# Performance work log

Measured on AMD Instinct MI355X. Metric: run time of the kernel, lower is better.

Reference implementation:

```python
import jax, jax.numpy as jnp
import numpy as np

N, F_IN, H, P, R = 50000, 384, 128, 128, 16
E = 500000


def _lin_params(key, fan_in, fan_out):
    k1, k2 = jax.random.split(key)
    s = 1.0 / np.sqrt(fan_in)
    W = jax.random.uniform(k1, (fan_in, fan_out), jnp.float32, -s, s)
    b = jax.random.uniform(k2, (fan_out,), jnp.float32, -s, s)
    return W, b


def setup_inputs() -> dict:
    key = jax.random.key(0)
    ks = jax.random.split(key, 16)
    x = jax.random.normal(ks[0], (N, F_IN), jnp.float32)
    edge_index = jax.random.randint(ks[1], (2, E), 0, N, jnp.int64)
    W_gcn1, b_gcn1 = _lin_params(ks[2], F_IN, H)
    W_ti, b_ti = _lin_params(ks[3], F_IN, F_IN)      # CrossFusion.text_info (384 -> dim=384)
    W_gi, b_gi = _lin_params(ks[4], H, F_IN)          # CrossFusion.graph_info (128 -> 384)
    W_v, b_v = _lin_params(ks[5], F_IN, F_IN)         # CrossFusion.value
    Wl1, bl1 = _lin_params(ks[6], F_IN, F_IN // 2)    # left_generator hidden
    Wl2, bl2 = _lin_params(ks[7], F_IN // 2, P * R)
    Wr1, br1 = _lin_params(ks[8], F_IN, F_IN // 2)    # right_generator hidden
    Wr2, br2 = _lin_params(ks[9], F_IN // 2, R * F_IN)
    W_gcn2, b_gcn2 = _lin_params(ks[10], P, H)        # fusion_gcn (128 -> 128)
    W_gp, b_gp = _lin_params(ks[11], P, P)            # graph_proj
    return dict(x=x, edge_index=edge_index, W_gcn1=W_gcn1, b_gcn1=b_gcn1,
                W_ti=W_ti, b_ti=b_ti, W_gi=W_gi, b_gi=b_gi, W_v=W_v, b_v=b_v,
                Wl1=Wl1, bl1=bl1, Wl2=Wl2, bl2=bl2, Wr1=Wr1, br1=br1, Wr2=Wr2, br2=br2,
                W_gcn2=W_gcn2, b_gcn2=b_gcn2, W_gp=W_gp, b_gp=b_gp)


def _gcn(x, W, b, src, dst, n):
    # PyG GCNConv: self-loops + symmetric degree normalization, aggregate at dst.
    xw = x @ W
    loop = jnp.arange(n, dtype=src.dtype)
    s = jnp.concatenate([src, loop])
    d = jnp.concatenate([dst, loop])
    deg = jax.ops.segment_sum(jnp.ones_like(d, dtype=xw.dtype), d, num_segments=n)
    dinv = jnp.where(deg > 0, jax.lax.rsqrt(deg), 0.0)
    norm = dinv[s] * dinv[d]                           # [E+N]
    out = jax.ops.segment_sum(norm[:, None] * xw[s], d, num_segments=n)
    return out + b


def _cross_fusion(text_feat, graph_feat, row, col, W_ti, b_ti, W_gi, b_gi, W_v, b_v):
    n, dim = text_feat.shape[0], W_ti.shape[1]
    t_info = text_feat @ W_ti + b_ti                   # [N, dim]
    g_info = graph_feat @ W_gi + b_gi                  # [N, dim]
    v = text_feat @ W_v + b_v                          # [N, dim]
    scores = jnp.sum(t_info[row] * g_info[col], axis=-1) / np.sqrt(dim)   # [E]
    m = jax.ops.segment_max(scores, row, num_segments=n)                  # scatter_softmax
    e = jnp.exp(scores - m[row])
    denom = jax.ops.segment_sum(e, row, num_segments=n)
    attn = e / denom[row]
    out = jax.ops.segment_sum(attn[:, None] * v[col], row, num_segments=n)
    return out + text_feat


def _forward(x, edge_index, W_gcn1, b_gcn1, W_ti, b_ti, W_gi, b_gi, W_v, b_v,
             Wl1, bl1, Wl2, bl2, Wr1, br1, Wr2, br2, W_gcn2, b_gcn2, W_gp, b_gp):
    src, dst = edge_index[0], edge_index[1]
    n = x.shape[0]
    g_emb = _gcn(x, W_gcn1, b_gcn1, src, dst, n)
    x_fused = _cross_fusion(x, g_emb, src, dst, W_ti, b_ti, W_gi, b_gi, W_v, b_v)
    # N > 40000 -> low-rank chunked projection (chunking is pure batching; vectorize)
    left = (jax.nn.relu(x_fused @ Wl1 + bl1) @ Wl2 + bl2).reshape(n, P, R)
    right = (jax.nn.relu(x_fused @ Wr1 + br1) @ Wr2 + br2).reshape(n, R, F_IN)
    temp = jnp.einsum('nrf,nf->nr', right, x)
    p_t = jnp.einsum('npr,nr->np', left, temp)         # [N, P]
    g2 = _gcn(p_t, W_gcn2, b_gcn2, src, dst, n)        # dropout is identity in eval
    p_g = g2 @ W_gp + b_gp
    p_t = p_t / jnp.maximum(jnp.linalg.norm(p_t, axis=-1, keepdims=True), 1e-12)
    p_g = p_g / jnp.maximum(jnp.linalg.norm(p_g, axis=-1, keepdims=True), 1e-12)
    alignment = jnp.sum(p_t * p_g, axis=1)
    return alignment, p_t, p_g, g2


def reference(x, edge_index, W_gcn1, b_gcn1, W_ti, b_ti, W_gi, b_gi, W_v, b_v,
              Wl1, bl1, Wl2, bl2, Wr1, br1, Wr2, br2, W_gcn2, b_gcn2, W_gp, b_gp):
    return _forward(x, edge_index, W_gcn1, b_gcn1, W_ti, b_ti, W_gi, b_gi, W_v, b_v,
                    Wl1, bl1, Wl2, bl2, Wr1, br1, Wr2, br2, W_gcn2, b_gcn2, W_gp, b_gp)
```

## Files before the change

kernel.cpp:

```cpp
#include <hip/hip_runtime.h>

typedef unsigned int u32;
typedef unsigned short u16;
typedef short s16x8 __attribute__((ext_vector_type(8)));
typedef u16 u16x8 __attribute__((ext_vector_type(8)));
typedef float f32x4 __attribute__((ext_vector_type(4)));

#define FIN 384
#define HD  128
#define PD  128
#define RD  16

#define GLOAD16(g, l)                                                          \
  __builtin_amdgcn_global_load_lds(                                            \
      (const __attribute__((address_space(1))) void*)(g),                      \
      (__attribute__((address_space(3))) void*)(l), 16, 0, 0)

__device__ __forceinline__ u16 f2bf(float f) {
  u32 u = __float_as_uint(f);
  u32 r = (u + 0x7fffu + ((u >> 16) & 1u)) >> 16;
  return (u16)r;
}
__device__ __forceinline__ float bf2f(u16 h) {
  return __uint_as_float(((u32)h) << 16);
}

struct CvtEnt { const float* s; u16* d; int K, N, mode, blk0; };
struct CvtDesc { CvtEnt e[12]; int n; };

__global__ void cvt_all_k(CvtDesc dsc) {
  int b = blockIdx.x;
  int ei = 0;
  while (ei + 1 < dsc.n && dsc.e[ei + 1].blk0 <= b) ++ei;
  CvtEnt E = dsc.e[ei];
  int i = (b - E.blk0) * 256 + (int)threadIdx.x;
  int tot = E.K * E.N;
  if (i >= tot) return;
  float v;
  if (E.mode == 0) {
    int c = i / E.K, k = i - c * E.K;
    v = E.s[(size_t)k * E.N + c];
  } else if (E.mode == 1) {
    v = E.s[i];
  } else {
    int q = i / 384, f = i - q * 384;
    v = E.s[(size_t)(q >> 4) * 6144 + (q & 15) * 384 + f];
  }
  E.d[i] = f2bf(v);
}

__global__ void hist_k(const int* __restrict__ src, const int* __restrict__ dst,
                       u32* __restrict__ cnt, int n, int E) {
  int i = blockIdx.x * 256 + threadIdx.x;
  if (i < E) {
    atomicAdd(&cnt[src[i]], 1u);
    atomicAdd(&cnt[n + dst[i]], 1u);
  }
}

__global__ __launch_bounds__(1024)
void scanA_k(const u32* __restrict__ cnt, u32* __restrict__ off,
             u32* __restrict__ bsum, int n2) {
  __shared__ u32 sh[1024];
  int i = blockIdx.x * 1024 + (int)threadIdx.x;
  u32 v = (i < n2) ? cnt[i] : 0u;
  sh[threadIdx.x] = v;
  __syncthreads();
  for (int s = 1; s < 1024; s <<= 1) {
    u32 t = (threadIdx.x >= (u32)s) ? sh[threadIdx.x - s] : 0u;
    __syncthreads();
    sh[threadIdx.x] += t;
    __syncthreads();
  }
  if (i < n2) off[i] = sh[threadIdx.x] - v;
  if (threadIdx.x == 1023) bsum[blockIdx.x] = sh[1023];
}

__global__ void scanB_k(u32* __restrict__ bsum, int nb) {
  int l = threadIdx.x;
  u32 carry = 0u;
  for (int base = 0; base < nb; base += 64) {
    u32 v = (base + l < nb) ? bsum[base + l] : 0u;
    for (int s = 1; s < 64; s <<= 1) {
      u32 t = __shfl_up(v, s);
      if (l >= s) v += t;
    }
    if (base + l < nb) bsum[base + l] = v + carry;
    carry += __shfl(v, 63);
  }
}

__global__ __launch_bounds__(1024)
void scanC_k(u32* __restrict__ off, u32* __restrict__ cur,
             const u32* __restrict__ bsum, int n2) {
  int b = blockIdx.x;
  int i = b * 1024 + (int)threadIdx.x;
  if (i >= n2) return;
  u32 add = (b > 0) ? bsum[b - 1] : 0u;
  u32 o = off[i] + add;
  off[i] = o;
  cur[i] = o;
}

__global__ void fill_k(const int* __restrict__ src, const int* __restrict__ dst,
                       u32* __restrict__ cur, u32* __restrict__ adj, int n, int E) {
  int i = blockIdx.x * 256 + threadIdx.x;
  if (i >= E) return;
  int s = src[i], d = dst[i];
  u32 ps = atomicAdd(&cur[s], 1u);
  adj[ps] = (u32)d;
  u32 pd = atomicAdd(&cur[n + d], 1u);
  adj[pd] = (u32)s;
}

__global__ void dinv_k(const u32* __restrict__ cd, float* __restrict__ dinv, int n) {
  int i = blockIdx.x * 256 + threadIdx.x;
  if (i < n) dinv[i] = 1.0f / sqrtf((float)(cd[i] + 1u));
}

template <int WF32, int WBF>
__global__ void gcn_agg_k(const u16* __restrict__ xw, const float* __restrict__ dinv,
                          const u32* __restrict__ off, const u32* __restrict__ cnt,
                          const u32* __restrict__ nbr, const float* __restrict__ bias,
                          float* __restrict__ outf, u16* __restrict__ outb, int n) {
  int node = (blockIdx.x * blockDim.x + threadIdx.x) >> 6;
  int lane = threadIdx.x & 63;
  if (node >= n) return;
  float di = dinv[node];
  ushort2 v = ((const ushort2*)(xw + (size_t)node * HD))[lane];
  float ax = di * di * bf2f(v.x), ay = di * di * bf2f(v.y);
  u32 i = off[node], end = i + cnt[node];
  for (; i + 2 <= end; i += 2) {
    int s0 = (int)nbr[i], s1 = (int)nbr[i + 1];
    float w0 = di * dinv[s0], w1 = di * dinv[s1];
    ushort2 u0 = ((const ushort2*)(xw + (size_t)s0 * HD))[lane];
    ushort2 u1 = ((const ushort2*)(xw + (size_t)s1 * HD))[lane];
    ax = fmaf(w0, bf2f(u0.x), ax);
    ay = fmaf(w0, bf2f(u0.y), ay);
    ax = fmaf(w1, bf2f(u1.x), ax);
    ay = fmaf(w1, bf2f(u1.y), ay);
  }
  if (i < end) {
    int s0 = (int)nbr[i];
    float w0 = di * dinv[s0];
    ushort2 u0 = ((const ushort2*)(xw + (size_t)s0 * HD))[lane];
    ax = fmaf(w0, bf2f(u0.x), ax);
    ay = fmaf(w0, bf2f(u0.y), ay);
  }
  float2 b = ((const float2*)bias)[lane];
  ax += b.x; ay += b.y;
  if (WF32) ((float2*)(outf + (size_t)node * HD))[lane] = make_float2(ax, ay);
  if (WBF) {
    ushort2 ob; ob.x = f2bf(ax); ob.y = f2bf(ay);
    ((ushort2*)(outb + (size_t)node * HD))[lane] = ob;
  }
}

__global__ void attn_fused_k(const u32* __restrict__ off, const u32* __restrict__ cnt,
                             const u32* __restrict__ adj,
                             const u16* __restrict__ ti, int TS,
                             const u16* __restrict__ gi, int GS,
                             const u16* __restrict__ vmat, int VS,
                             const u16* __restrict__ xb,
                             float* __restrict__ scores,
                             u16* __restrict__ xf, int n) {
  int node = (blockIdx.x * blockDim.x + threadIdx.x) >> 6;
  int lane = threadIdx.x & 63;
  if (node >= n) return;
  u32 o = off[node], c = cnt[node];
  u32 end = o + c;
  float acc[6] = {0.f, 0.f, 0.f, 0.f, 0.f, 0.f};
  if (c > 0) {
    const u16* tp = ti + (size_t)node * TS;
    float tf[6];
#pragma unroll
    for (int q = 0; q < 3; ++q) {
      ushort2 tv = *(const ushort2*)(tp + q * 128 + lane * 2);
      tf[q * 2] = bf2f(tv.x);
      tf[q * 2 + 1] = bf2f(tv.y);
    }
    const float sc = 0.05103103630798288f;
    float mx = -1e30f;
    u32 i = o;
    for (; i + 2 <= end; i += 2) {
      int d0 = (int)adj[i], d1 = (int)adj[i + 1];
      const u16* g0 = gi + (size_t)d0 * GS;
      const u16* g1 = gi + (size_t)d1 * GS;
      float dot0 = 0.f, dot1 = 0.f;
#pragma unroll
      for (int q = 0; q < 3; ++q) {
        ushort2 a = *(const ushort2*)(g0 + q * 128 + lane * 2);
        ushort2 b = *(const ushort2*)(g1 + q * 128 + lane * 2);
        dot0 = fmaf(tf[q * 2], bf2f(a.x), dot0);
        dot0 = fmaf(tf[q * 2 + 1], bf2f(a.y), dot0);
        dot1 = fmaf(tf[q * 2], bf2f(b.x), dot1);
        dot1 = fmaf(tf[q * 2 + 1], bf2f(b.y), dot1);
      }
#pragma unroll
      for (int s2 = 32; s2 >= 1; s2 >>= 1) {
        dot0 += __shfl_xor(dot0, s2);
        dot1 += __shfl_xor(dot1, s2);
      }
      dot0 *= sc; dot1 *= sc;
      if (lane == 0) { scores[i] = dot0; scores[i + 1] = dot1; }
      mx = fmaxf(mx, fmaxf(dot0, dot1));
    }
    if (i < end) {
      int d0 = (int)adj[i];
      const u16* g0 = gi + (size_t)d0 * GS;
      float dot0 = 0.f;
#pragma unroll
      for (int q = 0; q < 3; ++q) {
        ushort2 a = *(const ushort2*)(g0 + q * 128 + lane * 2);
        dot0 = fmaf(tf[q * 2], bf2f(a.x), dot0);
        dot0 = fmaf(tf[q * 2 + 1], bf2f(a.y), dot0);
      }
#pragma unroll
      for (int s2 = 32; s2 >= 1; s2 >>= 1) dot0 += __shfl_xor(dot0, s2);
      dot0 *= sc;
      if (lane == 0) scores[i] = dot0;
      mx = fmaxf(mx, dot0);
    }
    float den = 0.f;
    for (u32 k = o + lane; k < end; k += 64) den += expf(scores[k] - mx);
#pragma unroll
    for (int s2 = 32; s2 >= 1; s2 >>= 1) den += __shfl_xor(den, s2);
    float invden = 1.0f / den;
    i = o;
    for (; i + 2 <= end; i += 2) {
      int d0 = (int)adj[i], d1 = (int)adj[i + 1];
      float w0 = expf(scores[i] - mx) * invden;
      float w1 = expf(scores[i + 1] - mx) * invden;
      const u16* v0 = vmat + (size_t)d0 * VS;
      const u16* v1 = vmat + (size_t)d1 * VS;
#pragma unroll
      for (int q = 0; q < 3; ++q) {
        ushort2 a = *(const ushort2*)(v0 + q * 128 + lane * 2);
        ushort2 b = *(const ushort2*)(v1 + q * 128 + lane * 2);
        acc[q * 2]     = fmaf(w0, bf2f(a.x), acc[q * 2]);
        acc[q * 2 + 1] = fmaf(w0, bf2f(a.y), acc[q * 2 + 1]);
        acc[q * 2]     = fmaf(w1, bf2f(b.x), acc[q * 2]);
        acc[q * 2 + 1] = fmaf(w1, bf2f(b.y), acc[q * 2 + 1]);
      }
    }
    if (i < end) {
      int d0 = (int)adj[i];
      float w0 = expf(scores[i] - mx) * invden;
      const u16* v0 = vmat + (size_t)d0 * VS;
#pragma unroll
      for (int q = 0; q < 3; ++q) {
        ushort2 a = *(const ushort2*)(v0 + q * 128 + lane * 2);
        acc[q * 2]     = fmaf(w0, bf2f(a.x), acc[q * 2]);
        acc[q * 2 + 1] = fmaf(w0, bf2f(a.y), acc[q * 2 + 1]);
      }
    }
  }
  const u16* xp = xb + (size_t)node * FIN;
  u16* op = xf + (size_t)node * FIN;
#pragma unroll
  for (int q = 0; q < 3; ++q) {
    ushort2 xv = *(const ushort2*)(xp + q * 128 + lane * 2);
    ushort2 ov;
    ov.x = f2bf(acc[q * 2] + bf2f(xv.x));
    ov.y = f2bf(acc[q * 2 + 1] + bf2f(xv.y));
    *(ushort2*)(op + q * 128 + lane * 2) = ov;
  }
}

template <int EPI, int OUTBF>
__global__ __launch_bounds__(256)
void mgemm_k(const u16* __restrict__ Abf, int As, const u16* __restrict__ WT,
             const float* __restrict__ bias, const float* __restrict__ bias_b, int bsplit,
             void* __restrict__ Cp, u16* __restrict__ Cbf2,
             float* __restrict__ tmp, int M, int K, int Nc) {
  __shared__ u16 Albuf[2][128 * 32];
  __shared__ u16 Blbuf[2][128 * 32];
  const int t = threadIdx.x;
  const int lane = t & 63;
  const int wave = t >> 6;
  const int wr = wave >> 1, wc = wave & 1;
  const int row0 = blockIdx.y * 128;
  const int col0 = blockIdx.x * 128;
  const int sr = t >> 2;
  const int sk = (t & 3) * 8;
  const int nt = K >> 5;

  f32x4 acc[4][4] = {};

  auto stage = [&](int buf, int k0) {
#pragma unroll
    for (int h = 0; h < 2; ++h) {
      int ar = row0 + h * 64 + sr;
      if (ar >= M) ar = M - 1;
      GLOAD16(Abf + (size_t)ar * As + k0 + sk, &Albuf[buf][h * 2048 + wave * 512]);
    }
#pragma unroll
    for (int h = 0; h < 2; ++h) {
      int bc = col0 + h * 64 + sr;
      if (bc >= Nc) bc = Nc - 1;
      GLOAD16(WT + (size_t)bc * K + k0 + sk, &Blbuf[buf][h * 2048 + wave * 512]);
    }
  };

  stage(0, 0);
  int buf = 0;
  for (int tk = 0; tk < nt; ++tk) {
    __syncthreads();
    if (tk + 1 < nt) stage(buf ^ 1, (tk + 1) << 5);
    const u16* Al = Albuf[buf];
    const u16* Bl = Blbuf[buf];
    s16x8 a[4], b[4];
#pragma unroll
    for (int m = 0; m < 4; ++m)
      a[m] = *(const s16x8*)(Al + (wr * 64 + m * 16 + (lane & 15)) * 32 + (lane >> 4) * 8);
#pragma unroll
    for (int j = 0; j < 4; ++j)
      b[j] = *(const s16x8*)(Bl + (wc * 64 + j * 16 + (lane & 15)) * 32 + (lane >> 4) * 8);
#pragma unroll
    for (int m = 0; m < 4; ++m)
#pragma unroll
      for (int j = 0; j < 4; ++j)
        acc[m][j] = __builtin_amdgcn_mfma_f32_16x16x32_bf16(a[m], b[j], acc[m][j], 0, 0, 0);
    buf ^= 1;
  }

  if constexpr (EPI <= 2) {
#pragma unroll
    for (int m = 0; m < 4; ++m) {
      int rbase = row0 + wr * 64 + m * 16 + (lane >> 4) * 4;
#pragma unroll
      for (int j = 0; j < 4; ++j) {
        int col = col0 + wc * 64 + j * 16 + (lane & 15);
        if (col >= Nc) continue;
        float bv = 0.f;
        if (EPI >= 1) bv = (col < bsplit) ? bias[col] : bias_b[col - bsplit];
#pragma unroll
        for (int r = 0; r < 4; ++r) {
          int row = rbase + r;
          if (row >= M) continue;
          float v = acc[m][j][r] + bv;
          if (EPI == 2) v = fmaxf(v, 0.f);
          if (OUTBF) ((u16*)Cp)[(size_t)row * Nc + col] = f2bf(v);
          else       ((float*)Cp)[(size_t)row * Nc + col] = v;
        }
      }
    }
  } else if constexpr (EPI == 6) {
#pragma unroll
    for (int m = 0; m < 4; ++m) {
      int rbase = row0 + wr * 64 + m * 16 + (lane >> 4) * 4;
#pragma unroll
      for (int j = 0; j < 4; ++j) {
        int col = col0 + wc * 64 + j * 16 + (lane & 15);
        if (col < 2 * FIN) {
          float bv = (col < bsplit) ? bias[col] : bias_b[col - bsplit];
#pragma unroll
          for (int r = 0; r < 4; ++r) {
            int row = rbase + r;
            if (row >= M) continue;
            ((u16*)Cp)[(size_t)row * (2 * FIN) + col] = f2bf(acc[m][j][r] + bv);
          }
        } else {
          int c2 = col - 2 * FIN;
#pragma unroll
          for (int r = 0; r < 4; ++r) {
            int row = rbase + r;
            if (row >= M) continue;
            Cbf2[(size_t)row * HD + c2] = f2bf(acc[m][j][r]);
          }
        }
      }
    }
  } else {
#pragma unroll
    for (int m = 0; m < 4; ++m) {
#pragma unroll
      for (int r = 0; r < 4; ++r) {
        int row = row0 + wr * 64 + m * 16 + (lane >> 4) * 4 + r;
        float tv = (row < M) ? tmp[(size_t)row * RD + (lane & 15)] : 0.f;
#pragma unroll
        for (int j = 0; j < 4; ++j) {
          float s = (acc[m][j][r] + bias[col0 + wc * 64 + j * 16 + (lane & 15)]) * tv;
          s += __shfl_xor(s, 1); s += __shfl_xor(s, 2);
          s += __shfl_xor(s, 4); s += __shfl_xor(s, 8);
          if ((lane & 15) == 0 && row < M) {
            int p = (col0 + wc * 64 + j * 16) >> 4;
            ((float*)Cp)[(size_t)row * PD + p] = s;
            Cbf2[(size_t)row * PD + p] = f2bf(s);
          }
        }
      }
    }
  }
}

#define VM6  asm volatile("s_waitcnt vmcnt(6)" ::: "memory")
#define VM0  asm volatile("s_waitcnt vmcnt(0)" ::: "memory")
#define VMNOP
#define BARR asm volatile("s_barrier" ::: "memory")

__global__ __launch_bounds__(512)
void ygemm8_k(const u16* __restrict__ X, const u16* __restrict__ QT,
              const u16* __restrict__ Ar, float* __restrict__ tmpP, int M) {
  __shared__ u16 Al[2][16384];
  __shared__ u16 Bl[2][16384];
  const int t = threadIdx.x;
  const int lane = t & 63;
  const int wave = t >> 6;
  const int wr = wave >> 2;
  const int wcn = wave & 3;
  const int row0 = blockIdx.y * 256;
  const int col0 = blockIdx.x * 256;

  const int srow = t >> 3;
  const int sgk  = (((t & 7) ^ (srow & 7)) << 3);
  const int sdst = t * 8;

  const int pc0 = (((lane >> 4)) ^ (lane & 7)) << 3;
  const int pc1 = ((((lane >> 4) + 4)) ^ (lane & 7)) << 3;
  const int arow = (wr * 128 + (lane & 15)) << 6;
  const int brow = (wcn * 64 + (lane & 15)) << 6;

  f32x4 acc[8][4] = {};
  s16x8 a[4][2], b[4][2];

#define STGA8(bf, h, kt) do {                                                  \
    int r0_ = row0 + (h) * 128 + srow;                                         \
    int r1_ = r0_ + 64;                                                        \
    if (r0_ >= M) r0_ = M - 1;                                                 \
    if (r1_ >= M) r1_ = M - 1;                                                 \
    GLOAD16(X + (size_t)r0_ * 384 + (kt) * 64 + sgk, &Al[bf][(h) * 8192 + sdst]);        \
    GLOAD16(X + (size_t)r1_ * 384 + (kt) * 64 + sgk, &Al[bf][(h) * 8192 + 4096 + sdst]); \
  } while (0)

#define STGB8(bf, h, kt) do {                                                  \
    int c0_ = col0 + (h) * 128 + srow;                                         \
    GLOAD16(QT + (size_t)c0_ * 384 + (kt) * 64 + sgk, &Bl[bf][(h) * 8192 + sdst]);       \
    GLOAD16(QT + (size_t)(c0_ + 64) * 384 + (kt) * 64 + sgk,                   \
            &Bl[bf][(h) * 8192 + 4096 + sdst]);                                \
  } while (0)

#define LDA8(bf, mh) do {                                                      \
    _Pragma("unroll") for (int m2_ = 0; m2_ < 4; ++m2_) {                      \
      const u16* p_ = &Al[bf][arow + ((mh) * 4 + m2_) * 1024];                 \
      a[m2_][0] = *(const s16x8*)(p_ + pc0);                                   \
      a[m2_][1] = *(const s16x8*)(p_ + pc1);                                   \
    }                                                                          \
  } while (0)

#define LDB8(bf, jh) do {                                                      \
    _Pragma("unroll") for (int j2_ = 0; j2_ < 2; ++j2_) {                      \
      const u16* p_ = &Bl[bf][brow + ((jh) * 2 + j2_) * 1024];                 \
      b[(jh) * 2 + j2_][0] = *(const s16x8*)(p_ + pc0);                        \
      b[(jh) * 2 + j2_][1] = *(const s16x8*)(p_ + pc1);                        \
    }                                                                          \
  } while (0)

#define MQ8(mh, jh) do {                                                       \
    __builtin_amdgcn_s_setprio(1);                                             \
    _Pragma("unroll") for (int m2_ = 0; m2_ < 4; ++m2_)                        \
      _Pragma("unroll") for (int j2_ = 0; j2_ < 2; ++j2_)                      \
        _Pragma("unroll") for (int ks_ = 0; ks_ < 2; ++ks_)                    \
          acc[(mh) * 4 + m2_][(jh) * 2 + j2_] =                                \
              __builtin_amdgcn_mfma_f32_16x16x32_bf16(                         \
                  a[m2_][ks_], b[(jh) * 2 + j2_][ks_],                         \
                  acc[(mh) * 4 + m2_][(jh) * 2 + j2_], 0, 0, 0);               \
    __builtin_amdgcn_s_setprio(0);                                             \
  } while (0)

  STGA8(0, 0, 0); STGA8(0, 1, 0); STGB8(0, 0, 0); STGB8(0, 1, 0);
  STGA8(1, 0, 1); STGB8(1, 0, 1); STGB8(1, 1, 1);
  VM6; BARR;

#define ITER8(i, VMP3, VMP7, DOSTG)                                                          \
   LDA8(0,0); LDB8(0,0); STGA8(1,1,2*(i)+1);                   BARR; MQ8(0,0); BARR;  \
   LDB8(0,1);                                                  BARR; MQ8(0,1); BARR;  \
   LDA8(0,1); if (DOSTG) STGB8(0,0,2*(i)+2);                   BARR; MQ8(1,0); BARR;  \
   if (DOSTG) { STGB8(0,1,2*(i)+2); STGA8(0,0,2*(i)+2); } VMP3; BARR; MQ8(1,1); BARR; \
   LDA8(1,0); LDB8(1,0); if (DOSTG) STGA8(0,1,2*(i)+2);        BARR; MQ8(0,0); BARR;  \
   LDB8(1,1);                                                  BARR; MQ8(0,1); BARR;  \
   LDA8(1,1); if (DOSTG) STGB8(1,0,2*(i)+3);                   BARR; MQ8(1,0); BARR;  \
   if (DOSTG) { STGB8(1,1,2*(i)+3); STGA8(1,0,2*(i)+3); } VMP7; BARR; MQ8(1,1); BARR;

  ITER8(0, VM6, VM6, 1)
  ITER8(1, VM6, VM6, 1)
  ITER8(2, VM0, VMNOP, 0)

  const int h0 = (col0 >> 4) + wcn * 4;
  float s[8][4];
#pragma unroll
  for (int m = 0; m < 8; ++m) {
#pragma unroll
    for (int rr = 0; rr < 4; ++rr) {
      int row = row0 + wr * 128 + m * 16 + (lane >> 4) * 4 + rr;
      int rc = row < M ? row : M - 1;
      ushort4 arv = *(const ushort4*)(Ar + (size_t)rc * 384 + h0);
      s[m][rr] = bf2f(arv.x) * acc[m][0][rr] + bf2f(arv.y) * acc[m][1][rr] +
                 bf2f(arv.z) * acc[m][2][rr] + bf2f(arv.w) * acc[m][3][rr];
    }
  }

  __syncthreads();
  float* redA = (float*)&Al[0][0];
  float* redB = redA + 4096;
  const int r16 = lane & 15;
  const int rlb = wr * 128 + (lane >> 4) * 4;
  if (wcn & 1) {
    float* red = (wcn == 1) ? redA : redB;
#pragma unroll
    for (int m = 0; m < 8; ++m)
#pragma unroll
      for (int rr = 0; rr < 4; ++rr)
        red[(rlb + m * 16 + rr) * 16 + r16] = s[m][rr];
  }
  __syncthreads();
  if (!(wcn & 1)) {
    float* red = (wcn == 0) ? redA : redB;
#pragma unroll
    for (int m = 0; m < 8; ++m)
#pragma unroll
      for (int rr = 0; rr < 4; ++rr)
        s[m][rr] += red[(rlb + m * 16 + rr) * 16 + r16];
  }
  __syncthreads();
  if (wcn == 2) {
#pragma unroll
    for (int m = 0; m < 8; ++m)
#pragma unroll
      for (int rr = 0; rr < 4; ++rr)
        redA[(rlb + m * 16 + rr) * 16 + r16] = s[m][rr];
  }
  __syncthreads();
  if (wcn == 0) {
    float* slice = tmpP + (size_t)blockIdx.x * M * RD;
#pragma unroll
    for (int m = 0; m < 8; ++m)
#pragma unroll
      for (int rr = 0; rr < 4; ++rr) {
        int row = row0 + rlb + m * 16 + rr;
        if (row < M)
          slice[(size_t)row * RD + r16] =
              s[m][rr] + redA[(rlb + m * 16 + rr) * 16 + r16];
      }
  }
#undef STGA8
#undef STGB8
#undef LDA8
#undef LDB8
#undef MQ8
#undef ITER8
}

__global__ void combine_k(const float* __restrict__ tmpP, float* __restrict__ temp,
                          size_t sl, int tot4) {
  int i = blockIdx.x * 256 + threadIdx.x;
  if (i >= tot4) return;
  float4 s = ((const float4*)(tmpP + 12 * sl))[i];
#pragma unroll
  for (int c = 0; c < 12; ++c) {
    float4 p = ((const float4*)(tmpP + (size_t)c * sl))[i];
    s.x += p.x; s.y += p.y; s.z += p.z; s.w += p.w;
  }
  ((float4*)temp)[i] = s;
}

__global__ void final_k(float* __restrict__ out, int n) {
  int node = (blockIdx.x * blockDim.x + threadIdx.x) >> 6;
  int lane = threadIdx.x & 63;
  if (node >= n) return;
  float* pt = out + n + (size_t)node * PD;
  float* pg = out + n + (size_t)n * PD + (size_t)node * PD;
  float2 t = ((float2*)pt)[lane];
  float2 g = ((float2*)pg)[lane];
  float tt = t.x * t.x + t.y * t.y;
  float gg = g.x * g.x + g.y * g.y;
  float tg = t.x * g.x + t.y * g.y;
#pragma unroll
  for (int s = 32; s >= 1; s >>= 1) {
    tt += __shfl_xor(tt, s);
    gg += __shfl_xor(gg, s);
    tg += __shfl_xor(tg, s);
  }
  float invt = 1.0f / fmaxf(sqrtf(tt), 1e-12f);
  float invg = 1.0f / fmaxf(sqrtf(gg), 1e-12f);
  ((float2*)pt)[lane] = make_float2(t.x * invt, t.y * invt);
  ((float2*)pg)[lane] = make_float2(g.x * invg, g.y * invg);
  if (lane == 0) out[node] = tg * invt * invg;
}

struct MgArgs {
  const u16* A; int As; const u16* WT;
  const float* b; const float* b2; int bsplit;
  void* C; u16* C2; float* tmp;
  int M, K, Nc;
};
template <int EPI, int OUTBF>
static void mg(const MgArgs& a, hipStream_t s) {
  dim3 grid((a.Nc + 127) / 128, (a.M + 127) / 128);
  mgemm_k<EPI, OUTBF><<<grid, 256, 0, s>>>(a.A, a.As, a.WT, a.b, a.b2, a.bsplit,
                                           a.C, a.C2, a.tmp, a.M, a.K, a.Nc);
}

extern "C" void kernel_launch(void* const* d_in, const int* in_sizes, int n_in,
                              void* d_out, int out_size, void* d_ws, size_t ws_size,
                              hipStream_t stream) {
  const float* x      = (const float*)d_in[0];
  const int*   ei     = (const int*)d_in[1];
  const float* W_gcn1 = (const float*)d_in[2];
  const float* b_gcn1 = (const float*)d_in[3];
  const float* W_ti   = (const float*)d_in[4];
  const float* b_ti   = (const float*)d_in[5];
  const float* W_gi   = (const float*)d_in[6];
  const float* b_gi   = (const float*)d_in[7];
  const float* W_v    = (const float*)d_in[8];
  const float* b_v    = (const float*)d_in[9];
  const float* Wl1    = (const float*)d_in[10];
  const float* bl1    = (const float*)d_in[11];
  const float* Wl2    = (const float*)d_in[12];
  const float* bl2    = (const float*)d_in[13];
  const float* Wr1    = (const float*)d_in[14];
  const float* br1    = (const float*)d_in[15];
  const float* Wr2    = (const float*)d_in[16];
  const float* br2    = (const float*)d_in[17];
  const float* W_gcn2 = (const float*)d_in[18];
  const float* b_gcn2 = (const float*)d_in[19];
  const float* W_gp   = (const float*)d_in[20];
  const float* b_gp   = (const float*)d_in[21];

  const int n = in_sizes[0] / FIN;
  const int E = in_sizes[1] / 2;
  const int* src = ei;
  const int* dst = ei + E;

  char* wsp = (char*)d_ws;
  auto carve = [&](size_t bytes) -> void* {
    void* p = (void*)wsp;
    wsp += (bytes + 255) & ~(size_t)255;
    return p;
  };
  u32* cnt      = (u32*)carve((size_t)2 * n * 4);
  u32* off      = (u32*)carve((size_t)2 * n * 4);
  u32* cur      = (u32*)carve((size_t)2 * n * 4);
  u32* bsum     = (u32*)carve(512);
  u32* adj      = (u32*)carve((size_t)2 * E * 4);
  float* dinv   = (float*)carve((size_t)n * 4);
  float* scores = (float*)carve((size_t)E * 4);
  float* temp   = (float*)carve((size_t)n * RD * 4);

  u16* xbf    = (u16*)carve((size_t)n * FIN * 2);
  u16* tvbf   = (u16*)carve((size_t)n * 2 * FIN * 2);
  u16* bufHbf = (u16*)carve((size_t)n * HD * 2);
  u16* gembf  = (u16*)carve((size_t)n * HD * 2);
  u16* ptbf   = (u16*)carve((size_t)n * PD * 2);
  u16* g2bf   = (u16*)carve((size_t)n * HD * 2);

  u16* gibf   = (u16*)carve((size_t)n * FIN * 2);
  u16* xfbf   = (u16*)carve((size_t)n * FIN * 2);
  size_t tmpP_bytes = (size_t)13 * n * RD * 4;
  size_t overlay    = (size_t)2 * n * FIN * 2;
  carve(tmpP_bytes > overlay ? tmpP_bytes - overlay : 0);
  float* tmpP = (float*)gibf;

  u16* WtvT   = (u16*)carve((size_t)2 * FIN * FIN * 2);
  u16* WgcnT  = (u16*)carve((size_t)HD * FIN * 2);
  u16* WgiT   = (u16*)carve((size_t)FIN * HD * 2);
  u16* WlrT   = (u16*)carve((size_t)FIN * FIN * 2);
  u16* Wl2T   = (u16*)carve((size_t)2048 * 192 * 2);
  u16* QT     = (u16*)carve((size_t)3072 * FIN * 2);
  u16* BrT    = (u16*)carve((size_t)RD * FIN * 2);
  u16* Wgcn2T = (u16*)carve((size_t)HD * PD * 2);
  u16* WgpT   = (u16*)carve((size_t)PD * PD * 2);

  u16* lrbf = tvbf;

  float* out    = (float*)d_out;
  float* pt_raw = out + n;
  float* pg_raw = out + n + (size_t)n * PD;
  float* g2     = out + n + (size_t)2 * n * PD;

  CvtDesc dsc;
  int nent = 0, blk = 0;
  auto addent = [&](const float* s, u16* d, int K, int N, int mode) {
    dsc.e[nent] = {s, d, K, N, mode, blk};
    blk += (K * N + 255) / 256;
    ++nent;
  };
  addent(x,      xbf,    n * FIN, 1, 1);
  addent(W_ti,   WtvT,   FIN, FIN, 0);
  addent(W_v,    WtvT + (size_t)FIN * FIN, FIN, FIN, 0);
  addent(W_gcn1, WgcnT,  FIN, HD,  0);
  addent(W_gi,   WgiT,   HD,  FIN, 0);
  addent(Wl1,    WlrT,   FIN, 192, 0);
  addent(Wr1,    WlrT + (size_t)192 * FIN, FIN, 192, 0);
  addent(Wl2,    Wl2T,   192, 2048, 0);
  addent(Wr2,    QT,     FIN, 3072, 2);
  addent(br2,    BrT,    RD * FIN, 1, 1);
  addent(W_gcn2, Wgcn2T, PD, HD, 0);
  addent(W_gp,   WgpT,   PD, PD, 0);
  dsc.n = nent;
  cvt_all_k<<<blk, 256, 0, stream>>>(dsc);

  hipMemsetAsync(cnt, 0, (size_t)2 * n * 4, stream);
  hist_k<<<(E + 255) / 256, 256, 0, stream>>>(src, dst, cnt, n, E);
  int n2 = 2 * n;
  int nb = (n2 + 1023) / 1024;
  scanA_k<<<nb, 1024, 0, stream>>>(cnt, off, bsum, n2);
  scanB_k<<<1, 64, 0, stream>>>(bsum, nb);
  scanC_k<<<nb, 1024, 0, stream>>>(off, cur, bsum, n2);
  fill_k<<<(E + 255) / 256, 256, 0, stream>>>(src, dst, cur, adj, n, E);
  dinv_k<<<(n + 255) / 256, 256, 0, stream>>>(cnt + n, dinv, n);

  MgArgs a{};

  a = {xbf, FIN, WtvT, b_ti, b_v, FIN, tvbf, bufHbf, nullptr, n, FIN, 896};
  mg<6, 1>(a, stream);
  gcn_agg_k<0, 1><<<(n + 3) / 4, 256, 0, stream>>>(bufHbf, dinv, off + n, cnt + n, adj,
                                                   b_gcn1, nullptr, gembf, n);

  a = {gembf, HD, WgiT, b_gi, nullptr, 1 << 30, gibf, nullptr, nullptr, n, HD, FIN};
  mg<1, 1>(a, stream);
  attn_fused_k<<<(n + 3) / 4, 256, 0, stream>>>(off, cnt, adj, tvbf, 2 * FIN, gibf, FIN,
                                                tvbf + FIN, 2 * FIN, xbf, scores, xfbf, n);

  a = {xfbf, FIN, WlrT, bl1, br1, 192, lrbf, nullptr, nullptr, n, FIN, FIN};
  mg<2, 1>(a, stream);

  a = {xbf, FIN, BrT, nullptr, nullptr, 1 << 30, tmpP + (size_t)12 * n * RD, nullptr,
       nullptr, n, FIN, RD};
  mg<0, 0>(a, stream);
  ygemm8_k<<<dim3(12, (n + 255) / 256), 512, 0, stream>>>(xbf, QT, lrbf + 192, tmpP, n);
  combine_k<<<(n * RD / 4 + 255) / 256, 256, 0, stream>>>(tmpP, temp, (size_t)n * RD,
                                                          n * RD / 4);

  a = {lrbf, FIN, Wl2T, bl2, nullptr, 1 << 30, pt_raw, ptbf, temp, n, 192, PD * RD};
  mg<4, 0>(a, stream);

  a = {ptbf, PD, Wgcn2T, nullptr, nullptr, 1 << 30, bufHbf, nullptr, nullptr, n, PD, HD};
  mg<0, 1>(a, stream);
  gcn_agg_k<1, 1><<<(n + 3) / 4, 256, 0, stream>>>(bufHbf, dinv, off + n, cnt + n, adj,
                                                   b_gcn2, g2, g2bf, n);
  a = {g2bf, HD, WgpT, b_gp, nullptr, 1 << 30, pg_raw, nullptr, nullptr, n, HD, PD};
  mg<1, 0>(a, stream);

  final_k<<<(n + 3) / 4, 256, 0, stream>>>(out, n);
}
```

Baseline: 964.4 us.

## Replace left-generator GEMM with dedicated 256x256 tiled kernel plus gather pass

Moves the Wl2 projection (K=192 zero-padded to 256) off the generic GEMM onto a dedicated 512-thread kernel with 256x256 tiles, double-buffered LDS and direct global-to-LDS loads. The epilogue contracts with temp and writes per-column-tile partial slices, and a new gather kernel rearranges them into p_t in float and bf16. This targets the heaviest GEMM with a tile shape meant for better data reuse. In exchange it adds a padded K that does extra work on zeros and another kernel launch plus a round trip through scratch memory.

```diff
diff --git a/kernel.cpp b/kernel.cpp
--- a/kernel.cpp
+++ b/kernel.cpp
@@ -42,6 +42,9 @@
     v = E.s[(size_t)k * E.N + c];
   } else if (E.mode == 1) {
     v = E.s[i];
+  } else if (E.mode == 3) {
+    int c = i / E.K, k = i - c * E.K;
+    v = (k < 192) ? E.s[(size_t)k * E.N + c] : 0.f;
   } else {
     int q = i / 384, f = i - q * 384;
     v = E.s[(size_t)(q >> 4) * 6144 + (q & 15) * 384 + f];
@@ -371,26 +374,24 @@
         }
       }
     }
-  } else {
-#pragma unroll
-    for (int m = 0; m < 4; ++m) {
-#pragma unroll
-      for (int r = 0; r < 4; ++r) {
-        int row = row0 + wr * 64 + m * 16 + (lane >> 4) * 4 + r;
-        float tv = (row < M) ? tmp[(size_t)row * RD + (lane & 15)] : 0.f;
-#pragma unroll
-        for (int j = 0; j < 4; ++j) {
-          float s = (acc[m][j][r] + bias[col0 + wc * 64 + j * 16 + (lane & 15)]) * tv;
-          s += __shfl_xor(s, 1); s += __shfl_xor(s, 2);
-          s += __shfl_xor(s, 4); s += __shfl_xor(s, 8);
-          if ((lane & 15) == 0 && row < M) {
-            int p = (col0 + wc * 64 + j * 16) >> 4;
-            ((float*)Cp)[(size_t)row * PD + p] = s;
-            Cbf2[(size_t)row * PD + p] = f2bf(s);
-          }
-        }
-      }
-    }
+  }
+}
+
+__global__ void ptgather_k(const float* __restrict__ ptP, float* __restrict__ pt,
+                           u16* __restrict__ ptb, int n) {
+  int g = blockIdx.x * 256 + threadIdx.x;
+  if (g >= n * 8) return;
+  int row = g >> 3, ct = g & 7;
+  const float* sp = ptP + ((size_t)ct * n + (size_t)row) * 16;
+  float* dp = pt + (size_t)row * PD + ct * 16;
+  u16* db = ptb + (size_t)row * PD + ct * 16;
+#pragma unroll
+  for (int q = 0; q < 4; ++q) {
+    float4 a = ((const float4*)sp)[q];
+    ((float4*)dp)[q] = a;
+    ushort4 oa;
+    oa.x = f2bf(a.x); oa.y = f2bf(a.y); oa.z = f2bf(a.z); oa.w = f2bf(a.w);
+    ((ushort4*)db)[q] = oa;
   }
 }
 
@@ -542,6 +543,77 @@
           slice[(size_t)row * RD + r16] =
               s[m][rr] + redA[(rlb + m * 16 + rr) * 16 + r16];
       }
+  }
+#undef STGA8
+#undef STGB8
+}
+
+__global__ __launch_bounds__(512)
+void lgemm8_k(const u16* __restrict__ X, const u16* __restrict__ WL,
+              const float* __restrict__ bl2, const float* __restrict__ temp,
+              float* __restrict__ ptP, int M) {
+  __shared__ u16 Al[2][16384];
+  __shared__ u16 Bl[2][16384];
+  const int t = threadIdx.x;
+  const int lane = t & 63;
+  const int wave = t >> 6;
+  const int wr = wave >> 2;
+  const int wcn = wave & 3;
+  const int row0 = blockIdx.y * 256;
+  const int col0 = blockIdx.x * 256;
+
+  const int srow = t >> 3;
+  const int sgk  = (((t & 7) ^ (srow & 7)) << 3);
+  const int sdst = t * 8;
+
+  const int pc0 = (((lane >> 4)) ^ (lane & 7)) << 3;
+  const int pc1 = ((((lane >> 4) + 4)) ^ (lane & 7)) << 3;
+  const int arow = (wr * 128 + (lane & 15)) << 6;
+  const int brow = (wcn * 64 + (lane & 15)) << 6;
+
+  f32x4 acc[8][4] = {};
+  s16x8 a[4][2], b[4][2];
+
+#define STGA8(bf, h, kt) do {                                                  \
+    int r0_ = row0 + (h) * 128 + srow;                                         \
+    int r1_ = r0_ + 64;                                                        \
+    if (r0_ >= M) r0_ = M - 1;                                                 \
+    if (r1_ >= M) r1_ = M - 1;                                                 \
+    GLOAD16(X + (size_t)r0_ * 384 + (kt) * 64 + sgk, &Al[bf][(h) * 8192 + sdst]);        \
+    GLOAD16(X + (size_t)r1_ * 384 + (kt) * 64 + sgk, &Al[bf][(h) * 8192 + 4096 + sdst]); \
+  } while (0)
+
+#define STGB8(bf, h, kt) do {                                                  \
+    int c0_ = col0 + (h) * 128 + srow;                                         \
+    GLOAD16(WL + (size_t)c0_ * 256 + (kt) * 64 + sgk, &Bl[bf][(h) * 8192 + sdst]);       \
+    GLOAD16(WL + (size_t)(c0_ + 64) * 256 + (kt) * 64 + sgk,                   \
+            &Bl[bf][(h) * 8192 + 4096 + sdst]);                                \
+  } while (0)
+
+  STGA8(0, 0, 0); STGA8(0, 1, 0); STGB8(0, 0, 0); STGB8(0, 1, 0);
+  STGA8(1, 0, 1); STGB8(1, 0, 1); STGB8(1, 1, 1);
+  VM6; BARR;
+
+  ITER8(0, VM6, VM6, 1)
+  ITER8(1, VM0, VMNOP, 0)
+
+  float* slice = ptP + (size_t)blockIdx.x * M * 16;
+#pragma unroll
+  for (int m = 0; m < 8; ++m) {
+#pragma unroll
+    for (int rr = 0; rr < 4; ++rr) {
+      int row = row0 + wr * 128 + m * 16 + (lane >> 4) * 4 + rr;
+      float tv = (row < M) ? temp[(size_t)row * RD + (lane & 15)] : 0.f;
+#pragma unroll
+      for (int j = 0; j < 4; ++j) {
+        int col = col0 + wcn * 64 + j * 16 + (lane & 15);
+        float s = (acc[m][j][rr] + bl2[col]) * tv;
+        s += __shfl_xor(s, 1); s += __shfl_xor(s, 2);
+        s += __shfl_xor(s, 4); s += __shfl_xor(s, 8);
+        if ((lane & 15) == 0 && row < M)
+          slice[(size_t)row * 16 + wcn * 4 + j] = s;
+      }
+    }
   }
 #undef STGA8
 #undef STGB8
@@ -660,12 +732,13 @@
   size_t overlay    = (size_t)2 * n * FIN * 2;
   carve(tmpP_bytes > overlay ? tmpP_bytes - overlay : 0);
   float* tmpP = (float*)gibf;
+  float* ptP  = tmpP;
 
   u16* WtvT   = (u16*)carve((size_t)2 * FIN * FIN * 2);
   u16* WgcnT  = (u16*)carve((size_t)HD * FIN * 2);
   u16* WgiT   = (u16*)carve((size_t)FIN * HD * 2);
   u16* WlrT   = (u16*)carve((size_t)FIN * FIN * 2);
-  u16* Wl2T   = (u16*)carve((size_t)2048 * 192 * 2);
+  u16* Wl2T   = (u16*)carve((size_t)2048 * 256 * 2);
   u16* QT     = (u16*)carve((size_t)3072 * FIN * 2);
   u16* BrT    = (u16*)carve((size_t)RD * FIN * 2);
   u16* Wgcn2T = (u16*)carve((size_t)HD * PD * 2);
@@ -692,7 +765,7 @@
   addent(W_gi,   WgiT,   HD,  FIN, 0);
   addent(Wl1,    WlrT,   FIN, 192, 0);
   addent(Wr1,    WlrT + (size_t)192 * FIN, FIN, 192, 0);
-  addent(Wl2,    Wl2T,   192, 2048, 0);
+  addent(Wl2,    Wl2T,   256, 2048, 3);
   addent(Wr2,    QT,     FIN, 3072, 2);
   addent(br2,    BrT,    RD * FIN, 1, 1);
   addent(W_gcn2, Wgcn2T, PD, HD, 0);
@@ -732,8 +805,8 @@
   combine_k<<<(n * RD / 4 + 255) / 256, 256, 0, stream>>>(tmpP, temp, (size_t)n * RD,
                                                           n * RD / 4);
 
-  a = {lrbf, FIN, Wl2T, bl2, nullptr, 1 << 30, pt_raw, ptbf, temp, n, 192, PD * RD};
-  mg<4, 0>(a, stream);
+  lgemm8_k<<<dim3(8, (n + 255) / 256), 512, 0, stream>>>(lrbf, Wl2T, bl2, temp, ptP, n);
+  ptgather_k<<<(n * 8 + 255) / 256, 256, 0, stream>>>(ptP, pt_raw, ptbf, n);
 
   a = {ptbf, PD, Wgcn2T, nullptr, nullptr, 1 << 30, bufHbf, nullptr, nullptr, n, PD, HD};
   mg<0, 1>(a, stream);
```

After: 1.029 ms. 6.7% more time.
